# Performance work log

Measured on AMD Instinct MI355X. Metric: run time of the kernel, lower is better.

## Reference

```python
import jax, jax.numpy as jnp
import numpy as np

LN_EPS = 1e-5   # torch nn.LayerNorm default eps
L2_EPS = 1e-12  # torch F.normalize default eps


def setup_inputs() -> dict:
    key = jax.random.key(0)
    k1, k2 = jax.random.split(key)
    b, c, h, w = 4, 256, 128, 256
    num_classes, num_prototype, proj_dim = 19, 10, 256
    x = jax.random.normal(k1, (b, c, h, w), dtype=jnp.float32)
    # trunc_normal_(std=0.02) approximated by normal * 0.02 (l2-normalized in fwd anyway)
    prototypes = jax.random.normal(k2, (num_classes, num_prototype, proj_dim), dtype=jnp.float32) * 0.02
    mask_norm_weight = jnp.ones((num_classes,), dtype=jnp.float32)
    mask_norm_bias = jnp.zeros((num_classes,), dtype=jnp.float32)
    return {"x": x, "prototypes": prototypes,
            "mask_norm_weight": mask_norm_weight, "mask_norm_bias": mask_norm_bias}


def _layer_norm(y, w, b):
    mu = jnp.mean(y, axis=-1, keepdims=True)
    var = jnp.var(y, axis=-1, keepdims=True)
    return (y - mu) * jax.lax.rsqrt(var + LN_EPS) * w + b


def reference(x, prototypes, mask_norm_weight, mask_norm_bias):
    b, c, h, w = x.shape
    # self.prototypes.data.copy_(l2_normalize(self.prototypes)) -- normalize over feature dim
    protos = prototypes / (jnp.linalg.norm(prototypes, axis=-1, keepdims=True) + L2_EPS)
    # rearrange 'b c h w -> (b h w) c'
    xf = x.transpose(0, 2, 3, 1).reshape(-1, c)           # [n, d]
    # cosine similarity: einsum('nd,kmd->nmk') then permute -> [n, k(classes), m(protos)]
    sim_mat = jnp.einsum('nd,kmd->nkm', xf, protos)       # [n, cls, proto]
    out_seg = jnp.max(sim_mat, axis=2)                    # amax over prototypes -> [n, cls]
    out_seg = _layer_norm(out_seg, mask_norm_weight, mask_norm_bias)
    # rearrange '(b h w) c -> b c h w'
    return out_seg.reshape(b, h, w, -1).transpose(0, 3, 1, 2)
```

## Files before the change

kernel.cpp:

```cpp
#include <hip/hip_runtime.h>


#define CC_   256
#define HW_   32768
#define NPIX_ 131072
#define NCLS_ 19
#define MBLK_ 128
#define SIMST_ 194

typedef __attribute__((ext_vector_type(8)))  short bf16x8;
typedef __attribute__((ext_vector_type(16))) float f32x16;
typedef __attribute__((ext_vector_type(2)))  float f32x2;
typedef __attribute__((ext_vector_type(4)))  unsigned int u32x4;
typedef __attribute__((ext_vector_type(2)))  unsigned int u32x2;

__device__ __forceinline__ void gll16(const void* g, void* l) {
  __builtin_amdgcn_global_load_lds((__attribute__((address_space(1))) void*)(g),
                                   (__attribute__((address_space(3))) void*)(l), 16, 0, 0);
}

#define SCHED() __builtin_amdgcn_sched_barrier(0)
#define BAR_LG() do {                                            \
  SCHED();                                                       \
  asm volatile("s_waitcnt lgkmcnt(0)" ::: "memory");             \
  __builtin_amdgcn_s_barrier();                                  \
  SCHED();                                                       \
} while (0)
#define BAR_VMLG(N) do {                                         \
  SCHED();                                                       \
  asm volatile("s_waitcnt vmcnt(" #N ") lgkmcnt(0)" ::: "memory"); \
  __builtin_amdgcn_s_barrier();                                  \
  SCHED();                                                       \
} while (0)

__global__ void prep_protos(const float* __restrict__ protos, char* __restrict__ Bp) {
  const int p = blockIdx.x;
  const int l = threadIdx.x;
  __shared__ float pn[256];
  float v[4] = {0.f, 0.f, 0.f, 0.f};
  float sq = 0.f;
  if (p < 190) {
    #pragma unroll
    for (int i = 0; i < 4; ++i) {
      v[i] = protos[p * 256 + l * 4 + i];
      sq += v[i] * v[i];
    }
  }
  #pragma unroll
  for (int off = 32; off > 0; off >>= 1) sq += __shfl_xor(sq, off, 64);
  const float scale = (p < 190) ? 1.0f / (sqrtf(sq) + 1e-12f) : 0.0f;
  #pragma unroll
  for (int i = 0; i < 4; ++i) pn[l * 4 + i] = v[i] * scale;
  __syncthreads();

  const int oct  = l >> 1;
  const int part = l & 1;
  unsigned int w[4];
  #pragma unroll
  for (int pr = 0; pr < 4; ++pr) {
    const float f0 = pn[oct * 8 + 2 * pr];
    const float f1 = pn[oct * 8 + 2 * pr + 1];
    const unsigned int u0 = __builtin_bit_cast(unsigned int, f0);
    const unsigned int u1 = __builtin_bit_cast(unsigned int, f1);
    if (part == 0) {
      w[pr] = (u1 & 0xFFFF0000u) | (u0 >> 16);
    } else {
      const float t0 = __builtin_bit_cast(float, u0 & 0xFFFF0000u);
      const float t1 = __builtin_bit_cast(float, u1 & 0xFFFF0000u);
      const unsigned int v0 = __builtin_bit_cast(unsigned int, f0 - t0);
      const unsigned int v1 = __builtin_bit_cast(unsigned int, f1 - t1);
      w[pr] = (v1 & 0xFFFF0000u) | (v0 >> 16);
    }
  }
  const int cc = oct >> 2, ks = (oct >> 1) & 1, ko = oct & 1;
  const int nt = p >> 5, cL = p & 31;
  const size_t a16 = (size_t)((((cc * 2 + ks) * 6 + nt) * 2 + part) * 64 + ko * 32 + cL);
  *(u32x4*)(Bp + a16 * 16) = (u32x4){w[0], w[1], w[2], w[3]};
}

__device__ __forceinline__ void stageA(char* Albase, const f32x2 (&aLd)[4],
                                       int ksw, int kow, int sub, int mtw, int r15w) {
  #pragma unroll
  for (int e = 0; e < 2; ++e) {
    unsigned int wh[2], wl[2];
    #pragma unroll
    for (int q = 0; q < 2; ++q) {
      const float f0 = aLd[2 * q][e];
      const float f1 = aLd[2 * q + 1][e];
      const unsigned int u0 = __builtin_bit_cast(unsigned int, f0);
      const unsigned int u1 = __builtin_bit_cast(unsigned int, f1);
      wh[q] = (u1 & 0xFFFF0000u) | (u0 >> 16);
      const float t0 = __builtin_bit_cast(float, u0 & 0xFFFF0000u);
      const float t1 = __builtin_bit_cast(float, u1 & 0xFFFF0000u);
      const unsigned int v0 = __builtin_bit_cast(unsigned int, f0 - t0);
      const unsigned int v1 = __builtin_bit_cast(unsigned int, f1 - t1);
      wl[q] = (v1 & 0xFFFF0000u) | (v0 >> 16);
    }
    const int slotH = ((ksw * 2 + 0) * 4 + mtw) * 64 + kow * 32 + e * 16 + r15w;
    const int slotL = ((ksw * 2 + 1) * 4 + mtw) * 64 + kow * 32 + e * 16 + r15w;
    *(u32x2*)(Albase + slotH * 16 + sub * 8) = (u32x2){wh[0], wh[1]};
    *(u32x2*)(Albase + slotL * 16 + sub * 8) = (u32x2){wl[0], wl[1]};
  }
}

__launch_bounds__(512, 4)
__global__ void gemm_kernel(const float* __restrict__ x, const char* __restrict__ Bp,
                            const float* __restrict__ mw, const float* __restrict__ mb,
                            float* __restrict__ out) {
  __shared__ __align__(16) char smem[65536];
  char* Albase = smem;
  char* Blbase = smem + 16384;

  const int tid  = threadIdx.x;
  const int wave = tid >> 6;
  const int lane = tid & 63;
  const int n0   = blockIdx.x * MBLK_;
  const int b    = n0 >> 15;
  const int hw0  = n0 & (HW_ - 1);
  const float* xb = x + (size_t)b * CC_ * HW_ + hw0;

  const int ksw = wave >> 2, kow = (wave >> 1) & 1, sub = wave & 1;
  const int mtw = lane >> 4, r15w = lane & 15;
  const float* xA = xb + (size_t)(wave * 4) * HW_ + 2 * lane;

  const int rowg = wave >> 1, colg = wave & 1;

  f32x16 acc[3];
  #pragma unroll
  for (int nt = 0; nt < 3; ++nt) acc[nt] = (f32x16)(0.0f);

  f32x2 aA[4], aB[4];

  #pragma unroll
  for (int i = 0; i < 3; ++i)
    gll16(Bp + (size_t)(tid + 512 * i) * 16, Blbase + (tid + 512 * i) * 16);
  SCHED();
  #pragma unroll
  for (int j = 0; j < 4; ++j) aA[j] = *(const f32x2*)(xA + (size_t)j * HW_);
  SCHED();
  #pragma unroll
  for (int j = 0; j < 4; ++j) aB[j] = *(const f32x2*)(xA + (size_t)(32 + j) * HW_);
  SCHED();
  stageA(Albase, aA, ksw, kow, sub, mtw, r15w);
  #pragma unroll
  for (int i = 0; i < 3; ++i)
    gll16(Bp + (size_t)(1536 + tid + 512 * i) * 16, Blbase + 24576 + (tid + 512 * i) * 16);
  BAR_LG();

  #pragma unroll
  for (int cc = 0; cc < 8; ++cc) {
    const int buf = cc & 1;
    if (cc + 2 < 8) {
      f32x2 (&dst)[4] = (cc & 1) ? aB : aA;
      const float* xn = xA + (size_t)((cc + 2) * 32) * HW_;
      #pragma unroll
      for (int j = 0; j < 4; ++j) dst[j] = *(const f32x2*)(xn + (size_t)j * HW_);
    }
    const char* Bq = Blbase + buf * 24576;
    #pragma unroll
    for (int ks = 0; ks < 2; ++ks) {
      const bf16x8 ah = *(const bf16x8*)(Albase + (size_t)((((ks * 2 + 0) * 4 + rowg) * 64 + lane) * 16));
      const bf16x8 al = *(const bf16x8*)(Albase + (size_t)((((ks * 2 + 1) * 4 + rowg) * 64 + lane) * 16));
      #pragma unroll
      for (int nt = 0; nt < 3; ++nt) {
        const int ntg = colg * 3 + nt;
        const bf16x8 bh = *(const bf16x8*)(Bq + (size_t)(((ks * 12 + ntg * 2 + 0) * 64 + lane) * 16));
        const bf16x8 bl = *(const bf16x8*)(Bq + (size_t)(((ks * 12 + ntg * 2 + 1) * 64 + lane) * 16));
        acc[nt] = __builtin_amdgcn_mfma_f32_32x32x16_bf16(ah, bh, acc[nt], 0, 0, 0);
        acc[nt] = __builtin_amdgcn_mfma_f32_32x32x16_bf16(al, bh, acc[nt], 0, 0, 0);
        acc[nt] = __builtin_amdgcn_mfma_f32_32x32x16_bf16(ah, bl, acc[nt], 0, 0, 0);
      }
    }
    BAR_LG();
    if (cc + 2 < 8) {
      #pragma unroll
      for (int i = 0; i < 3; ++i)
        gll16(Bp + (size_t)((cc + 2) * 1536 + tid + 512 * i) * 16,
              Blbase + buf * 24576 + (tid + 512 * i) * 16);
    }
    if (cc < 7) {
      f32x2 (&stg)[4] = (cc & 1) ? aA : aB;
      stageA(Albase, stg, ksw, kow, sub, mtw, r15w);
      if (cc < 6) BAR_VMLG(7);
      else        BAR_VMLG(0);
    }
  }

  float* sims = (float*)smem;
  #pragma unroll 1
  for (int r = 0; r < 2; ++r) {
    if ((rowg >> 1) == r) {
      const int srow = (rowg & 1) * 32;
      #pragma unroll
      for (int nt = 0; nt < 3; ++nt) {
        #pragma unroll
        for (int q = 0; q < 16; ++q) {
          const int row = (q & 3) + 8 * (q >> 2) + 4 * (lane >> 5);
          sims[(srow + row) * SIMST_ + (colg * 3 + nt) * 32 + (lane & 31)] = acc[nt][q];
        }
      }
    }
    __syncthreads();
    if (tid < 64) {
      float mx[NCLS_];
      #pragma unroll
      for (int k = 0; k < NCLS_; ++k) {
        const float* rp = sims + tid * SIMST_ + k * 10;
        const f32x2 v0 = *(const f32x2*)(rp + 0);
        const f32x2 v1 = *(const f32x2*)(rp + 2);
        const f32x2 v2 = *(const f32x2*)(rp + 4);
        const f32x2 v3 = *(const f32x2*)(rp + 6);
        const f32x2 v4 = *(const f32x2*)(rp + 8);
        float m01 = fmaxf(fmaxf(v0[0], v0[1]), fmaxf(v1[0], v1[1]));
        float m23 = fmaxf(fmaxf(v2[0], v2[1]), fmaxf(v3[0], v3[1]));
        mx[k] = fmaxf(fmaxf(m01, m23), fmaxf(v4[0], v4[1]));
      }
      float mu = 0.f;
      #pragma unroll
      for (int k = 0; k < NCLS_; ++k) mu += mx[k];
      mu *= (1.0f / NCLS_);
      float var = 0.f;
      #pragma unroll
      for (int k = 0; k < NCLS_; ++k) { const float d = mx[k] - mu; var += d * d; }
      var *= (1.0f / NCLS_);
      const float rstd = rsqrtf(var + 1e-5f);
      const int s = tid & 31;
      const int hw = hw0 + (2 * r + (tid >> 5)) * 32 + ((s & 15) << 1) + (s >> 4);
      #pragma unroll
      for (int k = 0; k < NCLS_; ++k) {
        out[((size_t)(b * NCLS_ + k) << 15) + hw] = (mx[k] - mu) * rstd * mw[k] + mb[k];
      }
    }
    __syncthreads();
  }
}

extern "C" void kernel_launch(void* const* d_in, const int* in_sizes, int n_in,
                              void* d_out, int out_size, void* d_ws, size_t ws_size,
                              hipStream_t stream) {
  const float* x      = (const float*)d_in[0];
  const float* protos = (const float*)d_in[1];
  const float* mw     = (const float*)d_in[2];
  const float* mb     = (const float*)d_in[3];
  float* out = (float*)d_out;
  char* Bp   = (char*)d_ws;

  prep_protos<<<192, 64, 0, stream>>>(protos, Bp);
  gemm_kernel<<<NPIX_ / MBLK_, 512, 0, stream>>>(x, Bp, mw, mb, out);
}
```

Measured before the change: 206.1 us.

## Halve workgroup to 4 waves, each computing two M tiles to reuse B fragments

The block drops from 8 waves to 4, and each wave now computes two 32-row M tiles against three N tiles. This lets each B fragment loaded from LDS feed two MFMA chains, halving B LDS reads per MFMA. A staging now writes full 16-byte LDS vectors instead of two 8-byte halves. In exchange each thread issues twice as many global loads, holds twice the accumulators, and the launch bounds change to (256, 2), which raises register pressure and reduces waves per CU.

```diff
diff --git a/kernel.cpp b/kernel.cpp
--- a/kernel.cpp
+++ b/kernel.cpp
@@ -12,7 +12,6 @@
 typedef __attribute__((ext_vector_type(16))) float f32x16;
 typedef __attribute__((ext_vector_type(2)))  float f32x2;
 typedef __attribute__((ext_vector_type(4)))  unsigned int u32x4;
-typedef __attribute__((ext_vector_type(2)))  unsigned int u32x2;
 
 __device__ __forceinline__ void gll16(const void* g, void* l) {
   __builtin_amdgcn_global_load_lds((__attribute__((address_space(1))) void*)(g),
@@ -78,13 +77,13 @@
   *(u32x4*)(Bp + a16 * 16) = (u32x4){w[0], w[1], w[2], w[3]};
 }
 
-__device__ __forceinline__ void stageA(char* Albase, const f32x2 (&aLd)[4],
-                                       int ksw, int kow, int sub, int mtw, int r15w) {
+__device__ __forceinline__ void stageA(char* Albase, const f32x2 (&aLd)[8],
+                                       int ksw, int kow, int mtw, int r15w) {
   #pragma unroll
   for (int e = 0; e < 2; ++e) {
-    unsigned int wh[2], wl[2];
+    unsigned int wh[4], wl[4];
     #pragma unroll
-    for (int q = 0; q < 2; ++q) {
+    for (int q = 0; q < 4; ++q) {
       const float f0 = aLd[2 * q][e];
       const float f1 = aLd[2 * q + 1][e];
       const unsigned int u0 = __builtin_bit_cast(unsigned int, f0);
@@ -98,12 +97,12 @@
     }
     const int slotH = ((ksw * 2 + 0) * 4 + mtw) * 64 + kow * 32 + e * 16 + r15w;
     const int slotL = ((ksw * 2 + 1) * 4 + mtw) * 64 + kow * 32 + e * 16 + r15w;
-    *(u32x2*)(Albase + slotH * 16 + sub * 8) = (u32x2){wh[0], wh[1]};
-    *(u32x2*)(Albase + slotL * 16 + sub * 8) = (u32x2){wl[0], wl[1]};
-  }
-}
-
-__launch_bounds__(512, 4)
+    *(u32x4*)(Albase + (size_t)slotH * 16) = (u32x4){wh[0], wh[1], wh[2], wh[3]};
+    *(u32x4*)(Albase + (size_t)slotL * 16) = (u32x4){wl[0], wl[1], wl[2], wl[3]};
+  }
+}
+
+__launch_bounds__(256, 2)
 __global__ void gemm_kernel(const float* __restrict__ x, const char* __restrict__ Bp,
                             const float* __restrict__ mw, const float* __restrict__ mb,
                             float* __restrict__ out) {
@@ -119,69 +118,77 @@
   const int hw0  = n0 & (HW_ - 1);
   const float* xb = x + (size_t)b * CC_ * HW_ + hw0;
 
-  const int ksw = wave >> 2, kow = (wave >> 1) & 1, sub = wave & 1;
+  const int ksw = wave >> 1, kow = wave & 1;
   const int mtw = lane >> 4, r15w = lane & 15;
-  const float* xA = xb + (size_t)(wave * 4) * HW_ + 2 * lane;
+  const float* xA = xb + (size_t)(wave * 8) * HW_ + 2 * lane;
 
   const int rowg = wave >> 1, colg = wave & 1;
 
-  f32x16 acc[3];
-  #pragma unroll
-  for (int nt = 0; nt < 3; ++nt) acc[nt] = (f32x16)(0.0f);
-
-  f32x2 aA[4], aB[4];
-
-  #pragma unroll
-  for (int i = 0; i < 3; ++i)
-    gll16(Bp + (size_t)(tid + 512 * i) * 16, Blbase + (tid + 512 * i) * 16);
+  f32x16 acc[6];
+  #pragma unroll
+  for (int i = 0; i < 6; ++i) acc[i] = (f32x16)(0.0f);
+
+  f32x2 aA[8], aB[8];
+
+  #pragma unroll
+  for (int i = 0; i < 6; ++i)
+    gll16(Bp + (size_t)(tid + 256 * i) * 16, Blbase + (tid + 256 * i) * 16);
   SCHED();
   #pragma unroll
-  for (int j = 0; j < 4; ++j) aA[j] = *(const f32x2*)(xA + (size_t)j * HW_);
+  for (int j = 0; j < 8; ++j) aA[j] = *(const f32x2*)(xA + (size_t)j * HW_);
   SCHED();
   #pragma unroll
-  for (int j = 0; j < 4; ++j) aB[j] = *(const f32x2*)(xA + (size_t)(32 + j) * HW_);
+  for (int j = 0; j < 8; ++j) aB[j] = *(const f32x2*)(xA + (size_t)(32 + j) * HW_);
   SCHED();
-  stageA(Albase, aA, ksw, kow, sub, mtw, r15w);
-  #pragma unroll
-  for (int i = 0; i < 3; ++i)
-    gll16(Bp + (size_t)(1536 + tid + 512 * i) * 16, Blbase + 24576 + (tid + 512 * i) * 16);
+  stageA(Albase, aA, ksw, kow, mtw, r15w);
+  #pragma unroll
+  for (int i = 0; i < 6; ++i)
+    gll16(Bp + (size_t)(1536 + tid + 256 * i) * 16, Blbase + 24576 + (tid + 256 * i) * 16);
   BAR_LG();
 
   #pragma unroll
   for (int cc = 0; cc < 8; ++cc) {
     const int buf = cc & 1;
     if (cc + 2 < 8) {
-      f32x2 (&dst)[4] = (cc & 1) ? aB : aA;
+      f32x2 (&dst)[8] = (cc & 1) ? aB : aA;
       const float* xn = xA + (size_t)((cc + 2) * 32) * HW_;
       #pragma unroll
-      for (int j = 0; j < 4; ++j) dst[j] = *(const f32x2*)(xn + (size_t)j * HW_);
+      for (int j = 0; j < 8; ++j) dst[j] = *(const f32x2*)(xn + (size_t)j * HW_);
     }
     const char* Bq = Blbase + buf * 24576;
     #pragma unroll
     for (int ks = 0; ks < 2; ++ks) {
-      const bf16x8 ah = *(const bf16x8*)(Albase + (size_t)((((ks * 2 + 0) * 4 + rowg) * 64 + lane) * 16));
-      const bf16x8 al = *(const bf16x8*)(Albase + (size_t)((((ks * 2 + 1) * 4 + rowg) * 64 + lane) * 16));
+      bf16x8 ah[2], al[2];
+      #pragma unroll
+      for (int m = 0; m < 2; ++m) {
+        const int mt = rowg * 2 + m;
+        ah[m] = *(const bf16x8*)(Albase + (size_t)((((ks * 2 + 0) * 4 + mt) * 64 + lane) * 16));
+        al[m] = *(const bf16x8*)(Albase + (size_t)((((ks * 2 + 1) * 4 + mt) * 64 + lane) * 16));
+      }
       #pragma unroll
       for (int nt = 0; nt < 3; ++nt) {
         const int ntg = colg * 3 + nt;
         const bf16x8 bh = *(const bf16x8*)(Bq + (size_t)(((ks * 12 + ntg * 2 + 0) * 64 + lane) * 16));
         const bf16x8 bl = *(const bf16x8*)(Bq + (size_t)(((ks * 12 + ntg * 2 + 1) * 64 + lane) * 16));
-        acc[nt] = __builtin_amdgcn_mfma_f32_32x32x16_bf16(ah, bh, acc[nt], 0, 0, 0);
-        acc[nt] = __builtin_amdgcn_mfma_f32_32x32x16_bf16(al, bh, acc[nt], 0, 0, 0);
-        acc[nt] = __builtin_amdgcn_mfma_f32_32x32x16_bf16(ah, bl, acc[nt], 0, 0, 0);
+        #pragma unroll
+        for (int m = 0; m < 2; ++m) {
+          acc[m * 3 + nt] = __builtin_amdgcn_mfma_f32_32x32x16_bf16(ah[m], bh, acc[m * 3 + nt], 0, 0, 0);
+          acc[m * 3 + nt] = __builtin_amdgcn_mfma_f32_32x32x16_bf16(al[m], bh, acc[m * 3 + nt], 0, 0, 0);
+          acc[m * 3 + nt] = __builtin_amdgcn_mfma_f32_32x32x16_bf16(ah[m], bl, acc[m * 3 + nt], 0, 0, 0);
+        }
       }
     }
     BAR_LG();
     if (cc + 2 < 8) {
       #pragma unroll
-      for (int i = 0; i < 3; ++i)
-        gll16(Bp + (size_t)((cc + 2) * 1536 + tid + 512 * i) * 16,
-              Blbase + buf * 24576 + (tid + 512 * i) * 16);
+      for (int i = 0; i < 6; ++i)
+        gll16(Bp + (size_t)((cc + 2) * 1536 + tid + 256 * i) * 16,
+              Blbase + buf * 24576 + (tid + 256 * i) * 16);
     }
     if (cc < 7) {
-      f32x2 (&stg)[4] = (cc & 1) ? aA : aB;
-      stageA(Albase, stg, ksw, kow, sub, mtw, r15w);
-      if (cc < 6) BAR_VMLG(7);
+      f32x2 (&stg)[8] = (cc & 1) ? aA : aB;
+      stageA(Albase, stg, ksw, kow, mtw, r15w);
+      if (cc < 6) BAR_VMLG(14);
       else        BAR_VMLG(0);
     }
   }
@@ -189,14 +196,16 @@
   float* sims = (float*)smem;
   #pragma unroll 1
   for (int r = 0; r < 2; ++r) {
-    if ((rowg >> 1) == r) {
-      const int srow = (rowg & 1) * 32;
-      #pragma unroll
-      for (int nt = 0; nt < 3; ++nt) {
+    if (rowg == r) {
+      #pragma unroll
+      for (int m = 0; m < 2; ++m) {
         #pragma unroll
-        for (int q = 0; q < 16; ++q) {
-          const int row = (q & 3) + 8 * (q >> 2) + 4 * (lane >> 5);
-          sims[(srow + row) * SIMST_ + (colg * 3 + nt) * 32 + (lane & 31)] = acc[nt][q];
+        for (int nt = 0; nt < 3; ++nt) {
+          #pragma unroll
+          for (int q = 0; q < 16; ++q) {
+            const int row = m * 32 + (q & 3) + 8 * (q >> 2) + 4 * (lane >> 5);
+            sims[row * SIMST_ + (colg * 3 + nt) * 32 + (lane & 31)] = acc[m * 3 + nt][q];
+          }
         }
       }
     }
@@ -224,8 +233,7 @@
       for (int k = 0; k < NCLS_; ++k) { const float d = mx[k] - mu; var += d * d; }
       var *= (1.0f / NCLS_);
       const float rstd = rsqrtf(var + 1e-5f);
-      const int s = tid & 31;
-      const int hw = hw0 + (2 * r + (tid >> 5)) * 32 + ((s & 15) << 1) + (s >> 4);
+      const int hw = hw0 + (2 * r + (tid >> 5)) * 32 + ((tid & 15) << 1) + ((tid >> 4) & 1);
       #pragma unroll
       for (int k = 0; k < NCLS_; ++k) {
         out[((size_t)(b * NCLS_ + k) << 15) + hw] = (mx[k] - mu) * rstd * mw[k] + mb[k];
@@ -246,5 +254,5 @@
   char* Bp   = (char*)d_ws;
 
   prep_protos<<<192, 64, 0, stream>>>(protos, Bp);
-  gemm_kernel<<<NPIX_ / MBLK_, 512, 0, stream>>>(x, Bp, mw, mb, out);
-}
+  gemm_kernel<<<NPIX_ / MBLK_, 256, 0, stream>>>(x, Bp, mw, mb, out);
+}
```

New measurement: 210.2 us. About the same (+2.0%).
